# Optimization experiments

Hardware: AMD Instinct MI355X
Metric: run time of the kernel (lower is better)

The kernel has to match this reference:

```python
import jax, jax.numpy as jnp
import numpy as np

EMBED = 2048
N_EXPERTS = 64
TOP_K = 8


def setup_inputs() -> dict:
    key = jax.random.key(0)
    k_x, k_w, k_b = jax.random.split(key, 3)
    inputs = jax.random.normal(k_x, (8, 4096, EMBED), dtype=jnp.float32)
    # nn.Linear(embed_size, num_experts): weight [E, D], bias [E]
    bound = 1.0 / np.sqrt(EMBED)
    W = jax.random.uniform(k_w, (N_EXPERTS, EMBED), dtype=jnp.float32, minval=-bound, maxval=bound)
    b = jax.random.uniform(k_b, (N_EXPERTS,), dtype=jnp.float32, minval=-bound, maxval=bound)
    return {"inputs": inputs, "W": W, "b": b}


def reference(inputs, W, b):
    # scores: [B, S, E]
    scores = jnp.einsum("bsd,ed->bse", inputs, W) + b
    topk_scores, indices = jax.lax.top_k(scores, TOP_K)  # [B,S,K]
    # scatter topk_scores into a zero mask (non-selected slots stay 0.0)
    onehot = jax.nn.one_hot(indices, N_EXPERTS, dtype=scores.dtype)  # [B,S,K,E]
    mask = jnp.einsum("bske,bsk->bse", onehot, topk_scores)
    router_output = jax.nn.softmax(mask, axis=-1)
    return (router_output, indices)
```

## Files before the change

kernel.cpp:

```cpp
#include <hip/hip_runtime.h>
#include <math.h>

#define N_TOKENS 32768
#define EMBED    2048
#define NEXP     64
#define TOPK     8
#define BM       64
#define BK       32
#define LSTR     36
#define D4       (EMBED / 4)

__global__ __launch_bounds__(256, 2)
void router_kernel(const float* __restrict__ x, const float* __restrict__ W,
                   const float* __restrict__ bias, float* __restrict__ out) {
  __shared__ float  xs[BM * LSTR];
  __shared__ float  ws[NEXP * LSTR];
  __shared__ double sc[BM * NEXP];

  const int tid = threadIdx.x;
  const int t0  = blockIdx.x * BM;
  const int ty  = tid >> 4;
  const int tx  = tid & 15;
  const int r0  = tid >> 3;
  const int c0  = tid & 7;
  const int r1  = r0 + 32;

  const float4* x4 = (const float4*)x;
  const float4* W4 = (const float4*)W;

  double acc[4][4];
#pragma unroll
  for (int i = 0; i < 4; ++i)
#pragma unroll
    for (int j = 0; j < 4; ++j) acc[i][j] = 0.0;

  float4 ax0 = x4[(size_t)(t0 + r0) * D4 + c0];
  float4 ax1 = x4[(size_t)(t0 + r1) * D4 + c0];
  float4 aw0 = W4[(size_t)r0 * D4 + c0];
  float4 aw1 = W4[(size_t)r1 * D4 + c0];

  const int nch = EMBED / BK;
  for (int ch = 0; ch < nch; ++ch) {
    *(float4*)&xs[r0 * LSTR + (c0 << 2)] = ax0;
    *(float4*)&xs[r1 * LSTR + (c0 << 2)] = ax1;
    *(float4*)&ws[r0 * LSTR + (c0 << 2)] = aw0;
    *(float4*)&ws[r1 * LSTR + (c0 << 2)] = aw1;
    __syncthreads();

    if (ch + 1 < nch) {
      const int ko = (ch + 1) * (BK / 4) + c0;
      ax0 = x4[(size_t)(t0 + r0) * D4 + ko];
      ax1 = x4[(size_t)(t0 + r1) * D4 + ko];
      aw0 = W4[(size_t)r0 * D4 + ko];
      aw1 = W4[(size_t)r1 * D4 + ko];
    }

#pragma unroll
    for (int kk = 0; kk < BK; kk += 4) {
      float4 av4[4], bv4[4];
#pragma unroll
      for (int i = 0; i < 4; ++i)
        av4[i] = *(const float4*)&xs[(ty + 16 * i) * LSTR + kk];
#pragma unroll
      for (int j = 0; j < 4; ++j)
        bv4[j] = *(const float4*)&ws[(tx + 16 * j) * LSTR + kk];

      float aa[4][4], bb[4][4];
#pragma unroll
      for (int i = 0; i < 4; ++i) {
        aa[i][0] = av4[i].x; aa[i][1] = av4[i].y; aa[i][2] = av4[i].z; aa[i][3] = av4[i].w;
        bb[i][0] = bv4[i].x; bb[i][1] = bv4[i].y; bb[i][2] = bv4[i].z; bb[i][3] = bv4[i].w;
      }
#pragma unroll
      for (int s = 0; s < 4; ++s) {
        double ad[4], bd[4];
#pragma unroll
        for (int i = 0; i < 4; ++i) { ad[i] = (double)aa[i][s]; bd[i] = (double)bb[i][s]; }
#pragma unroll
        for (int i = 0; i < 4; ++i)
#pragma unroll
          for (int j = 0; j < 4; ++j)
            acc[i][j] = fma(ad[i], bd[j], acc[i][j]);
      }
    }
    __syncthreads();
  }

#pragma unroll
  for (int i = 0; i < 4; ++i)
#pragma unroll
    for (int j = 0; j < 4; ++j)
      sc[(ty + 16 * i) * NEXP + tx + 16 * j] = acc[i][j];
  __syncthreads();

  float* rout = out;
  float* iout = out + (size_t)N_TOKENS * NEXP;
  const int lane = tid & 63;
  const int wv   = tid >> 6;
  const double bl = (double)bias[lane];

  for (int tt = 0; tt < 16; ++tt) {
    const int t = wv * 16 + tt;
    const double orig = sc[t * NEXP + lane] + bl;
    double cur = orig;
    double vals[8];
    int    myidx  = 0;
    double mymask = 0.0;

#pragma unroll
    for (int r = 0; r < 8; ++r) {
      double v = cur;
      int    id = lane;
#pragma unroll
      for (int s2 = 1; s2 < 64; s2 <<= 1) {
        const double ov = __shfl_xor(v, s2);
        const int    oi = __shfl_xor(id, s2);
        if (ov > v || (ov == v && oi < id)) { v = ov; id = oi; }
      }
      vals[r] = v;
      if (lane == r)  myidx = id;
      if (lane == id) { mymask = orig; cur = -1e300; }
    }

    const double m = fmax(vals[0], 0.0);
    double Z = 56.0 * exp(-m);
#pragma unroll
    for (int r = 0; r < 8; ++r) Z += exp(vals[r] - m);
    const double p = exp(mymask - m) / Z;

    rout[(size_t)(t0 + t) * NEXP + lane] = (float)p;
    if (lane < TOPK) iout[(size_t)(t0 + t) * TOPK + lane] = (float)myidx;
  }
}

extern "C" void kernel_launch(void* const* d_in, const int* in_sizes, int n_in,
                              void* d_out, int out_size, void* d_ws, size_t ws_size,
                              hipStream_t stream) {
  const float* x = (const float*)d_in[0];
  const float* W = (const float*)d_in[1];
  const float* b = (const float*)d_in[2];
  router_kernel<<<N_TOKENS / BM, 256, 0, stream>>>(x, W, b, (float*)d_out);
}
```

Before: 576.1 us.

## Replace FP64 FMA GEMM with split-bf16 MFMA and FP64 fallback for near-ties

The scoring GEMM moves from FP64 scalar FMAs to bf16 MFMA 32x32x16 with a hi/lo split (three MFMAs per step) accumulating in fp32. Top-k now uses packed uint keys with the lane index in the low bits, giving one shuffle per step instead of two. Tokens whose top-9 score gaps fall below a threshold are recomputed exactly in FP64 from global memory so that index selection stays correct. This removes the costly FP64 ALU work. In exchange it adds a serial fallback path and a precision risk near ties.

```diff
diff --git a/kernel.cpp b/kernel.cpp
--- a/kernel.cpp
+++ b/kernel.cpp
@@ -6,130 +6,205 @@
 #define NEXP     64
 #define TOPK     8
 #define BM       64
-#define BK       32
-#define LSTR     36
+#define BK       64
 #define D4       (EMBED / 4)
+#define SCS      65
+#define THRESH   1e-4f
+
+typedef __attribute__((ext_vector_type(8)))  short short8;
+typedef __attribute__((ext_vector_type(16))) float f32x16;
+
+__device__ inline unsigned short bf16rne(float f) {
+  unsigned int fb = __float_as_uint(f);
+  return (unsigned short)((fb + 0x7FFFu + ((fb >> 16) & 1u)) >> 16);
+}
+
+__device__ inline void cvt8(float4 a, float4 b, short8& h, short8& l) {
+  float fs[8] = {a.x, a.y, a.z, a.w, b.x, b.y, b.z, b.w};
+#pragma unroll
+  for (int i = 0; i < 8; ++i) {
+    unsigned int hr = (__float_as_uint(fs[i]) + 0x7FFFu + ((__float_as_uint(fs[i]) >> 16) & 1u)) >> 16;
+    h[i] = (short)hr;
+    float hf = __uint_as_float(hr << 16);
+    l[i] = (short)bf16rne(fs[i] - hf);
+  }
+}
 
 __global__ __launch_bounds__(256, 2)
 void router_kernel(const float* __restrict__ x, const float* __restrict__ W,
                    const float* __restrict__ bias, float* __restrict__ out) {
-  __shared__ float  xs[BM * LSTR];
-  __shared__ float  ws[NEXP * LSTR];
-  __shared__ double sc[BM * NEXP];
-
-  const int tid = threadIdx.x;
-  const int t0  = blockIdx.x * BM;
-  const int ty  = tid >> 4;
-  const int tx  = tid & 15;
-  const int r0  = tid >> 3;
-  const int c0  = tid & 7;
-  const int r1  = r0 + 32;
+  __shared__ short xs_h[8 * 64 * 8], xs_l[8 * 64 * 8];
+  __shared__ short ws_h[8 * 64 * 8], ws_l[8 * 64 * 8];
+  __shared__ float sc[BM * SCS];
+  __shared__ double s_fix[NEXP];
+  __shared__ int s_list[BM];
+  __shared__ int s_cnt;
+
+  const int tid  = threadIdx.x;
+  const int t0   = blockIdx.x * BM;
+  const int lane = tid & 63;
+  const int w    = tid >> 6;
+  const int half = lane >> 5;
+  const int r5   = lane & 31;
+  const int tw   = (w & 1) * 32;
+  const int ew   = (w >> 1) * 32;
+
+  if (tid == 0) s_cnt = 0;
 
   const float4* x4 = (const float4*)x;
   const float4* W4 = (const float4*)W;
-
-  double acc[4][4];
-#pragma unroll
-  for (int i = 0; i < 4; ++i)
-#pragma unroll
-    for (int j = 0; j < 4; ++j) acc[i][j] = 0.0;
-
-  float4 ax0 = x4[(size_t)(t0 + r0) * D4 + c0];
-  float4 ax1 = x4[(size_t)(t0 + r1) * D4 + c0];
-  float4 aw0 = W4[(size_t)r0 * D4 + c0];
-  float4 aw1 = W4[(size_t)r1 * D4 + c0];
+  const int stok = tid & 63;
+  const float4* xrow = x4 + (size_t)(t0 + stok) * D4 + w * 4;
+  const float4* wrow = W4 + (size_t)stok * D4 + w * 4;
+
+  f32x16 acc;
+#pragma unroll
+  for (int i = 0; i < 16; ++i) acc[i] = 0.f;
+
+  float4 px[4], pw[4];
+#pragma unroll
+  for (int i = 0; i < 4; ++i) { px[i] = xrow[i]; pw[i] = wrow[i]; }
 
   const int nch = EMBED / BK;
   for (int ch = 0; ch < nch; ++ch) {
-    *(float4*)&xs[r0 * LSTR + (c0 << 2)] = ax0;
-    *(float4*)&xs[r1 * LSTR + (c0 << 2)] = ax1;
-    *(float4*)&ws[r0 * LSTR + (c0 << 2)] = aw0;
-    *(float4*)&ws[r1 * LSTR + (c0 << 2)] = aw1;
+    __syncthreads();
+    {
+      short8 h0, l0, h1, l1;
+      cvt8(px[0], px[1], h0, l0); cvt8(px[2], px[3], h1, l1);
+      *(short8*)&xs_h[((2 * w    ) * 64 + stok) * 8] = h0;
+      *(short8*)&xs_h[((2 * w + 1) * 64 + stok) * 8] = h1;
+      *(short8*)&xs_l[((2 * w    ) * 64 + stok) * 8] = l0;
+      *(short8*)&xs_l[((2 * w + 1) * 64 + stok) * 8] = l1;
+      cvt8(pw[0], pw[1], h0, l0); cvt8(pw[2], pw[3], h1, l1);
+      *(short8*)&ws_h[((2 * w    ) * 64 + stok) * 8] = h0;
+      *(short8*)&ws_h[((2 * w + 1) * 64 + stok) * 8] = h1;
+      *(short8*)&ws_l[((2 * w    ) * 64 + stok) * 8] = l0;
+      *(short8*)&ws_l[((2 * w + 1) * 64 + stok) * 8] = l1;
+    }
     __syncthreads();
 
     if (ch + 1 < nch) {
-      const int ko = (ch + 1) * (BK / 4) + c0;
-      ax0 = x4[(size_t)(t0 + r0) * D4 + ko];
-      ax1 = x4[(size_t)(t0 + r1) * D4 + ko];
-      aw0 = W4[(size_t)r0 * D4 + ko];
-      aw1 = W4[(size_t)r1 * D4 + ko];
-    }
-
-#pragma unroll
-    for (int kk = 0; kk < BK; kk += 4) {
-      float4 av4[4], bv4[4];
-#pragma unroll
-      for (int i = 0; i < 4; ++i)
-        av4[i] = *(const float4*)&xs[(ty + 16 * i) * LSTR + kk];
-#pragma unroll
-      for (int j = 0; j < 4; ++j)
-        bv4[j] = *(const float4*)&ws[(tx + 16 * j) * LSTR + kk];
-
-      float aa[4][4], bb[4][4];
-#pragma unroll
-      for (int i = 0; i < 4; ++i) {
-        aa[i][0] = av4[i].x; aa[i][1] = av4[i].y; aa[i][2] = av4[i].z; aa[i][3] = av4[i].w;
-        bb[i][0] = bv4[i].x; bb[i][1] = bv4[i].y; bb[i][2] = bv4[i].z; bb[i][3] = bv4[i].w;
-      }
-#pragma unroll
-      for (int s = 0; s < 4; ++s) {
-        double ad[4], bd[4];
-#pragma unroll
-        for (int i = 0; i < 4; ++i) { ad[i] = (double)aa[i][s]; bd[i] = (double)bb[i][s]; }
-#pragma unroll
-        for (int i = 0; i < 4; ++i)
-#pragma unroll
-          for (int j = 0; j < 4; ++j)
-            acc[i][j] = fma(ad[i], bd[j], acc[i][j]);
-      }
-    }
-    __syncthreads();
-  }
-
-#pragma unroll
-  for (int i = 0; i < 4; ++i)
-#pragma unroll
-    for (int j = 0; j < 4; ++j)
-      sc[(ty + 16 * i) * NEXP + tx + 16 * j] = acc[i][j];
+      const int off = (ch + 1) * (BK / 4);
+#pragma unroll
+      for (int i = 0; i < 4; ++i) { px[i] = xrow[off + i]; pw[i] = wrow[off + i]; }
+    }
+
+#pragma unroll
+    for (int s = 0; s < 4; ++s) {
+      const int kg = s * 2 + half;
+      short8 ah = *(const short8*)&xs_h[(kg * 64 + tw + r5) * 8];
+      short8 al = *(const short8*)&xs_l[(kg * 64 + tw + r5) * 8];
+      short8 bh = *(const short8*)&ws_h[(kg * 64 + ew + r5) * 8];
+      short8 bl = *(const short8*)&ws_l[(kg * 64 + ew + r5) * 8];
+      acc = __builtin_amdgcn_mfma_f32_32x32x16_bf16(ah, bh, acc, 0, 0, 0);
+      acc = __builtin_amdgcn_mfma_f32_32x32x16_bf16(ah, bl, acc, 0, 0, 0);
+      acc = __builtin_amdgcn_mfma_f32_32x32x16_bf16(al, bh, acc, 0, 0, 0);
+    }
+  }
+
+#pragma unroll
+  for (int reg = 0; reg < 16; ++reg) {
+    const int row = (reg & 3) + 8 * (reg >> 2) + 4 * half;
+    sc[(tw + row) * SCS + ew + r5] = acc[reg];
+  }
   __syncthreads();
 
   float* rout = out;
   float* iout = out + (size_t)N_TOKENS * NEXP;
-  const int lane = tid & 63;
-  const int wv   = tid >> 6;
-  const double bl = (double)bias[lane];
+  const float bias_l = bias[lane];
 
   for (int tt = 0; tt < 16; ++tt) {
-    const int t = wv * 16 + tt;
-    const double orig = sc[t * NEXP + lane] + bl;
-    double cur = orig;
-    double vals[8];
-    int    myidx  = 0;
-    double mymask = 0.0;
-
-#pragma unroll
-    for (int r = 0; r < 8; ++r) {
-      double v = cur;
-      int    id = lane;
+    const int t = w * 16 + tt;
+    const float orig = sc[t * SCS + lane] + bias_l;
+    unsigned int b = __float_as_uint(orig);
+    unsigned int u = b ^ (((unsigned int)((int)b >> 31)) | 0x80000000u);
+    const unsigned int key = (u & 0xFFFFFFC0u) | (63u - (unsigned int)lane);
+    unsigned int cur = key;
+    float fv[9];
+    int myidx = 0; bool sel = false; float morig = 0.f;
+
+#pragma unroll
+    for (int r = 0; r < 9; ++r) {
+      unsigned int v = cur;
 #pragma unroll
       for (int s2 = 1; s2 < 64; s2 <<= 1) {
-        const double ov = __shfl_xor(v, s2);
-        const int    oi = __shfl_xor(id, s2);
-        if (ov > v || (ov == v && oi < id)) { v = ov; id = oi; }
+        unsigned int o = (unsigned int)__shfl_xor((int)v, s2);
+        v = v > o ? v : o;
       }
-      vals[r] = v;
-      if (lane == r)  myidx = id;
-      if (lane == id) { mymask = orig; cur = -1e300; }
-    }
-
-    const double m = fmax(vals[0], 0.0);
-    double Z = 56.0 * exp(-m);
-#pragma unroll
-    for (int r = 0; r < 8; ++r) Z += exp(vals[r] - m);
-    const double p = exp(mymask - m) / Z;
-
-    rout[(size_t)(t0 + t) * NEXP + lane] = (float)p;
-    if (lane < TOPK) iout[(size_t)(t0 + t) * TOPK + lane] = (float)myidx;
+      unsigned int vb = (v & 0x80000000u) ? (v ^ 0x80000000u) : ~v;
+      fv[r] = __uint_as_float(vb);
+      if (r < 8) {
+        if (lane == r) myidx = 63 - (int)(v & 63u);
+        if (cur == v) { sel = true; morig = orig; cur = 0u; }
+      }
+    }
+
+    float ming = fv[0] - fv[1];
+#pragma unroll
+    for (int r = 1; r < 8; ++r) ming = fminf(ming, fv[r] - fv[r + 1]);
+
+    if (ming < THRESH) {
+      if (lane == 0) { int p = atomicAdd(&s_cnt, 1); s_list[p] = t; }
+    } else {
+      const float m = fmaxf(fv[0], 0.f);
+      float Z = 56.f * expf(-m);
+#pragma unroll
+      for (int r = 0; r < 8; ++r) Z += expf(fv[r] - m);
+      const float p = expf((sel ? morig : 0.f) - m) / Z;
+      rout[(size_t)(t0 + t) * NEXP + lane] = p;
+      if (lane < TOPK) iout[(size_t)(t0 + t) * TOPK + lane] = (float)myidx;
+    }
+  }
+
+  __syncthreads();
+  const int cnt = s_cnt;
+
+  for (int i = 0; i < cnt; ++i) {
+    const int t = s_list[i];
+    const int e = tid >> 2, sub = tid & 3;
+    const float4* xr = x4 + (size_t)(t0 + t) * D4 + sub * 128;
+    const float4* wr = W4 + (size_t)e * D4 + sub * 128;
+    double a0 = 0.0, a1 = 0.0;
+#pragma unroll 4
+    for (int m4 = 0; m4 < 128; m4 += 2) {
+      float4 xv = xr[m4], wv = wr[m4];
+      a0 = fma((double)xv.x, (double)wv.x, a0); a0 = fma((double)xv.y, (double)wv.y, a0);
+      a0 = fma((double)xv.z, (double)wv.z, a0); a0 = fma((double)xv.w, (double)wv.w, a0);
+      float4 xv2 = xr[m4 + 1], wv2 = wr[m4 + 1];
+      a1 = fma((double)xv2.x, (double)wv2.x, a1); a1 = fma((double)xv2.y, (double)wv2.y, a1);
+      a1 = fma((double)xv2.z, (double)wv2.z, a1); a1 = fma((double)xv2.w, (double)wv2.w, a1);
+    }
+    double a = a0 + a1;
+    a += __shfl_xor(a, 1); a += __shfl_xor(a, 2);
+    if (sub == 0) s_fix[e] = a + (double)bias[e];
+    __syncthreads();
+
+    if (tid < 64) {
+      const double orig = s_fix[lane];
+      double cur = orig, vals[8];
+      int myidx = 0; double mym = 0.0;
+#pragma unroll
+      for (int r = 0; r < 8; ++r) {
+        double v = cur; int id = lane;
+#pragma unroll
+        for (int s2 = 1; s2 < 64; s2 <<= 1) {
+          const double ov = __shfl_xor(v, s2);
+          const int    oi = __shfl_xor(id, s2);
+          if (ov > v || (ov == v && oi < id)) { v = ov; id = oi; }
+        }
+        vals[r] = v;
+        if (lane == r)  myidx = id;
+        if (lane == id) { mym = orig; cur = -1e300; }
+      }
+      const double m = fmax(vals[0], 0.0);
+      double Z = 56.0 * exp(-m);
+#pragma unroll
+      for (int r = 0; r < 8; ++r) Z += exp(vals[r] - m);
+      const double p = exp(mym - m) / Z;
+      rout[(size_t)(t0 + t) * NEXP + lane] = (float)p;
+      if (lane < TOPK) iout[(size_t)(t0 + t) * TOPK + lane] = (float)myidx;
+    }
+    __syncthreads();
   }
 }
 
```

New measurement: 568.1 us. Within noise of the previous version (-1.4%).
